# Kernel tuning notes

Measured on AMD Instinct MI355X. Metric: run time of the kernel, lower is better.

Reference implementation:

```python
import jax, jax.numpy as jnp
import numpy as np

IN_F = 4096
OUT_F = 4096
RANK = 16
N_BITS = 4
ALPHA = 1.0
GROUP = 128
Q_N = -(2 ** (N_BITS - 1))       # -8 for 4-bit signed
Q_P = 2 ** (N_BITS - 1) - 1      # +7
EPS = 1e-9


def setup_inputs() -> dict:
    key = jax.random.key(0)
    k0, k1, k2, k3, k4, k5 = jax.random.split(key, 6)
    x = jax.random.normal(k0, (8, 1024, IN_F), dtype=jnp.float32)
    w0 = jax.random.normal(k1, (OUT_F, IN_F), dtype=jnp.float32) * 0.02
    lora_a = jax.random.normal(k2, (RANK, IN_F), dtype=jnp.float32) * 0.02
    lora_b = jax.random.normal(k3, (OUT_F, RANK), dtype=jnp.float32) * 0.02
    num_groups = (OUT_F * IN_F) // GROUP
    q_scale = jnp.abs(jax.random.normal(k4, (num_groups,), dtype=jnp.float32)) * 0.01 + 0.005
    bias = jax.random.normal(k5, (OUT_F,), dtype=jnp.float32) * 0.01
    return {"x": x, "w0": w0, "lora_a": lora_a, "lora_b": lora_b,
            "q_scale": q_scale, "bias": bias}


def _quantize_weight(w0, lora_a, lora_b, q_scale):
    # LoRA merge: w_comb = w0 + alpha * (B @ A)   -> (OUT_F, IN_F)
    w_comb = w0 + ALPHA * (lora_b @ lora_a)
    num_groups = w_comb.size // GROUP
    w_g = w_comb.reshape(num_groups, GROUP)          # grouped view
    s = q_scale[:, None]                             # (G, 1) per-group scale
    w_scaled = w_g / (s + EPS)
    clamped = jnp.clip(w_scaled, Q_N, Q_P)
    q_int = jnp.round(clamped)
    w_q = (q_int * s).reshape(w_comb.shape)          # dequantized fake-quant weight
    return w_q


def reference(x, w0, lora_a, lora_b, q_scale, bias):
    w_q = _quantize_weight(w0, lora_a, lora_b, q_scale)
    # F.linear(x, w_q) + bias : (B, S, IN) @ (IN, OUT)
    return jnp.einsum('bsi,oi->bso', x, w_q) + bias
```

## Files before the change

kernel.cpp:

```cpp
#include <hip/hip_runtime.h>
#include <hip/hip_bf16.h>
#include <stdint.h>
#include <stddef.h>

#define IN_F   4096
#define OUT_F  4096
#define RANK   16
#define GROUP  128
#define M_TOT  8192
#define BM     128
#define BN     128
#define BK     32
#define NIT    (IN_F / BK)

typedef __bf16 bf16_t;
typedef __bf16 bf16x4 __attribute__((ext_vector_type(4)));
typedef __bf16 bf16x8 __attribute__((ext_vector_type(8)));
typedef float  f32x4  __attribute__((ext_vector_type(4)));

__device__ static inline void load_lds16(const void* g, void* l) {
  __builtin_amdgcn_global_load_lds(
      (const __attribute__((address_space(1))) unsigned int*)g,
      (__attribute__((address_space(3))) unsigned int*)l,
      16, 0, 0);
}

__global__ void __launch_bounds__(256)
quant_kernel(const float* __restrict__ w0, const float* __restrict__ la,
             const float* __restrict__ lb, const float* __restrict__ qs,
             bf16_t* __restrict__ wq)
{
  const int o = blockIdx.y;
  const int i = blockIdx.x * 1024 + threadIdx.x * 4;

  __shared__ float lbr[RANK];
  if (threadIdx.x < RANK) lbr[threadIdx.x] = lb[o * RANK + threadIdx.x];
  __syncthreads();

  const size_t off = (size_t)o * IN_F + i;
  const float4 w = *(const float4*)(w0 + off);
  float a0 = w.x, a1 = w.y, a2 = w.z, a3 = w.w;
  #pragma unroll
  for (int r = 0; r < RANK; ++r) {
    const float4 av = *(const float4*)(la + (size_t)r * IN_F + i);
    const float bv = lbr[r];
    a0 = fmaf(bv, av.x, a0);
    a1 = fmaf(bv, av.y, a1);
    a2 = fmaf(bv, av.z, a2);
    a3 = fmaf(bv, av.w, a3);
  }
  const float s   = qs[o * (IN_F / GROUP) + (i >> 7)];
  const float inv = 1.0f / (s + 1e-9f);
  const float q0 = rintf(fminf(fmaxf(a0 * inv, -8.0f), 7.0f)) * s;
  const float q1 = rintf(fminf(fmaxf(a1 * inv, -8.0f), 7.0f)) * s;
  const float q2 = rintf(fminf(fmaxf(a2 * inv, -8.0f), 7.0f)) * s;
  const float q3 = rintf(fminf(fmaxf(a3 * inv, -8.0f), 7.0f)) * s;
  bf16x4 v;
  v[0] = (bf16_t)q0; v[1] = (bf16_t)q1; v[2] = (bf16_t)q2; v[3] = (bf16_t)q3;
  *(bf16x4*)(wq + off) = v;
}

__global__ void __launch_bounds__(256)
castx_kernel(const float* __restrict__ x, bf16_t* __restrict__ xb)
{
  const size_t i = ((size_t)blockIdx.x * 256 + threadIdx.x) * 8;
  const float4 a = *(const float4*)(x + i);
  const float4 b = *(const float4*)(x + i + 4);
  bf16x8 v;
  v[0] = (bf16_t)a.x; v[1] = (bf16_t)a.y; v[2] = (bf16_t)a.z; v[3] = (bf16_t)a.w;
  v[4] = (bf16_t)b.x; v[5] = (bf16_t)b.y; v[6] = (bf16_t)b.z; v[7] = (bf16_t)b.w;
  *(bf16x8*)(xb + i) = v;
}

__global__ void __launch_bounds__(256, 3)
gemm_kernel(const bf16_t* __restrict__ A, const bf16_t* __restrict__ Bw,
            const float* __restrict__ bias, float* __restrict__ C)
{
  __shared__ __align__(16) bf16_t lA[2][BM * BK];
  __shared__ __align__(16) bf16_t lB[2][BN * BK];

  const int tid  = threadIdx.x;
  const int lane = tid & 63;
  const int lr   = lane & 15;
  const int quad = lane >> 4;
  const int wave = tid >> 6;

  const int m0 = blockIdx.y * BM;
  const int n0 = blockIdx.x * BN;

  const int srow = tid >> 2;
  const int scol = (tid & 3) * 8;

  const bf16_t* gA0 = A  + (size_t)(m0 + srow) * IN_F + scol;
  const bf16_t* gA1 = gA0 + (size_t)64 * IN_F;
  const bf16_t* gB0 = Bw + (size_t)(n0 + srow) * IN_F + scol;
  const bf16_t* gB1 = gB0 + (size_t)64 * IN_F;

  const int mb = (wave & 1) * 64;
  const int nb = (wave >> 1) * 64;

  f32x4 acc[4][4];
  #pragma unroll
  for (int i = 0; i < 4; ++i)
    #pragma unroll
    for (int j = 0; j < 4; ++j)
      acc[i][j] = (f32x4){0.f, 0.f, 0.f, 0.f};

  {
    char* dA = (char*)lA[0] + tid * 16;
    char* dB = (char*)lB[0] + tid * 16;
    load_lds16(gA0, dA);
    load_lds16(gA1, dA + 4096);
    load_lds16(gB0, dB);
    load_lds16(gB1, dB + 4096);
  }

  int buf = 0;
  for (int it = 0; it < NIT; ++it) {
    __syncthreads();

    if (it + 1 < NIT) {
      const int kt = (it + 1) * BK;
      char* dA = (char*)lA[buf ^ 1] + tid * 16;
      char* dB = (char*)lB[buf ^ 1] + tid * 16;
      load_lds16(gA0 + kt, dA);
      load_lds16(gA1 + kt, dA + 4096);
      load_lds16(gB0 + kt, dB);
      load_lds16(gB1 + kt, dB + 4096);
    }

    const bf16_t* sA = lA[buf];
    const bf16_t* sB = lB[buf];
    bf16x8 af[4], bfr[4];
    #pragma unroll
    for (int f = 0; f < 4; ++f)
      af[f]  = *(const bf16x8*)(sA + (mb + f * 16 + lr) * BK + quad * 8);
    #pragma unroll
    for (int f = 0; f < 4; ++f)
      bfr[f] = *(const bf16x8*)(sB + (nb + f * 16 + lr) * BK + quad * 8);

    #pragma unroll
    for (int fm = 0; fm < 4; ++fm)
      #pragma unroll
      for (int fn = 0; fn < 4; ++fn)
        acc[fm][fn] = __builtin_amdgcn_mfma_f32_16x16x32_bf16(
            af[fm], bfr[fn], acc[fm][fn], 0, 0, 0);

    buf ^= 1;
  }

  #pragma unroll
  for (int fn = 0; fn < 4; ++fn) {
    const int gn = n0 + nb + fn * 16 + lr;
    const float bv = bias[gn];
    #pragma unroll
    for (int fm = 0; fm < 4; ++fm) {
      const int gm = m0 + mb + fm * 16 + quad * 4;
      #pragma unroll
      for (int r = 0; r < 4; ++r)
        C[(size_t)(gm + r) * OUT_F + gn] = acc[fm][fn][r] + bv;
    }
  }
}

extern "C" void kernel_launch(void* const* d_in, const int* in_sizes, int n_in,
                              void* d_out, int out_size, void* d_ws, size_t ws_size,
                              hipStream_t stream) {
  const float* x    = (const float*)d_in[0];
  const float* w0   = (const float*)d_in[1];
  const float* la   = (const float*)d_in[2];
  const float* lb   = (const float*)d_in[3];
  const float* qs   = (const float*)d_in[4];
  const float* bias = (const float*)d_in[5];
  float* out = (float*)d_out;

  bf16_t* wq = (bf16_t*)d_ws;
  bf16_t* xb = (bf16_t*)((char*)d_ws + (size_t)OUT_F * IN_F * 2);

  quant_kernel<<<dim3(IN_F / 1024, OUT_F), 256, 0, stream>>>(w0, la, lb, qs, wq);
  castx_kernel<<<(M_TOT * IN_F) / (256 * 8), 256, 0, stream>>>(x, xb);
  gemm_kernel<<<dim3(OUT_F / BN, M_TOT / BM), 256, 0, stream>>>(xb, wq, bias, out);
}
```

Baseline: 599.5 us.

## Enlarge GEMM tiles to 256x256 with triple-buffered swizzled LDS pipeline

Reworks the bf16 MFMA GEMM to use 256x256 block tiles with 512 threads (8 waves), a three-stage LDS ring buffer loaded via global_load_lds, XOR-swizzled LDS layout to avoid bank conflicts, and a grid swizzle for L2 locality. The main loop is split into two half-steps, each with explicit waitcnt, barriers and setprio around its MFMA bursts, so global loads overlap compute. This is meant to raise arithmetic intensity and hide memory latency. In exchange it uses 96KB of dynamic LDS, more accumulator registers and hand-tuned synchronisation that could be fragile.

```diff
diff --git a/kernel.cpp b/kernel.cpp
--- a/kernel.cpp
+++ b/kernel.cpp
@@ -8,10 +8,14 @@
 #define RANK   16
 #define GROUP  128
 #define M_TOT  8192
-#define BM     128
-#define BN     128
+
+#define BM     256
+#define BN     256
 #define BK     32
 #define NIT    (IN_F / BK)
+#define HALF_B 16384
+#define TILE_B 32768
+#define LDS_B  (3 * TILE_B)
 
 typedef __bf16 bf16_t;
 typedef __bf16 bf16x4 __attribute__((ext_vector_type(4)));
@@ -72,90 +76,128 @@
   *(bf16x8*)(xb + i) = v;
 }
 
-__global__ void __launch_bounds__(256, 3)
+__global__ void __launch_bounds__(512, 2)
 gemm_kernel(const bf16_t* __restrict__ A, const bf16_t* __restrict__ Bw,
             const float* __restrict__ bias, float* __restrict__ C)
 {
-  __shared__ __align__(16) bf16_t lA[2][BM * BK];
-  __shared__ __align__(16) bf16_t lB[2][BN * BK];
+  extern __shared__ __align__(16) char smem[];
 
   const int tid  = threadIdx.x;
   const int lane = tid & 63;
   const int lr   = lane & 15;
   const int quad = lane >> 4;
-  const int wave = tid >> 6;
-
-  const int m0 = blockIdx.y * BM;
-  const int n0 = blockIdx.x * BN;
+  const int wid  = tid >> 6;
+  const int wm   = wid >> 2;
+  const int wn   = wid & 3;
+
+  const int bid = blockIdx.x;
+  const int swz = (bid & 7) * 64 + (bid >> 3);
+  const int m0  = (swz >> 4) * BM;
+  const int n0  = (swz & 15) * BN;
 
   const int srow = tid >> 2;
-  const int scol = (tid & 3) * 8;
-
+  const int scol = ((tid & 3) ^ ((tid >> 3) & 3)) * 8;
   const bf16_t* gA0 = A  + (size_t)(m0 + srow) * IN_F + scol;
-  const bf16_t* gA1 = gA0 + (size_t)64 * IN_F;
+  const bf16_t* gA1 = gA0 + (size_t)128 * IN_F;
   const bf16_t* gB0 = Bw + (size_t)(n0 + srow) * IN_F + scol;
-  const bf16_t* gB1 = gB0 + (size_t)64 * IN_F;
-
-  const int mb = (wave & 1) * 64;
-  const int nb = (wave >> 1) * 64;
-
-  f32x4 acc[4][4];
+  const bf16_t* gB1 = gB0 + (size_t)128 * IN_F;
+
+  const int rswz = (quad ^ ((lr >> 1) & 3)) * 16;
+  const int aOff = (wm * 128 + lr) * 64 + rswz;
+  const int bOff = (wn * 64  + lr) * 64 + rswz;
+
+  f32x4 acc[8][4];
   #pragma unroll
-  for (int i = 0; i < 4; ++i)
+  for (int i = 0; i < 8; ++i)
     #pragma unroll
     for (int j = 0; j < 4; ++j)
       acc[i][j] = (f32x4){0.f, 0.f, 0.f, 0.f};
 
   {
-    char* dA = (char*)lA[0] + tid * 16;
-    char* dB = (char*)lB[0] + tid * 16;
-    load_lds16(gA0, dA);
-    load_lds16(gA1, dA + 4096);
-    load_lds16(gB0, dB);
-    load_lds16(gB1, dB + 4096);
-  }
-
-  int buf = 0;
-  for (int it = 0; it < NIT; ++it) {
-    __syncthreads();
-
-    if (it + 1 < NIT) {
-      const int kt = (it + 1) * BK;
-      char* dA = (char*)lA[buf ^ 1] + tid * 16;
-      char* dB = (char*)lB[buf ^ 1] + tid * 16;
-      load_lds16(gA0 + kt, dA);
-      load_lds16(gA1 + kt, dA + 4096);
-      load_lds16(gB0 + kt, dB);
-      load_lds16(gB1 + kt, dB + 4096);
+    char* b0 = smem;
+    char* b1 = smem + TILE_B;
+    load_lds16(gA0,      b0 + tid * 16);
+    load_lds16(gA1,      b0 + tid * 16 + 8192);
+    load_lds16(gB0,      b0 + HALF_B + tid * 16);
+    load_lds16(gB1,      b0 + HALF_B + tid * 16 + 8192);
+    load_lds16(gA0 + BK, b1 + tid * 16);
+    load_lds16(gA1 + BK, b1 + tid * 16 + 8192);
+    load_lds16(gB0 + BK, b1 + HALF_B + tid * 16);
+    load_lds16(gB1 + BK, b1 + HALF_B + tid * 16 + 8192);
+    asm volatile("s_waitcnt vmcnt(4)" ::: "memory");
+    __builtin_amdgcn_s_barrier();
+  }
+
+  int rb = 0, wb = 2;
+  for (int t = 0; t < NIT; ++t) {
+    const char* rA   = smem + rb * TILE_B;
+    const char* rB   = rA + HALF_B;
+    char*       wbuf = smem + wb * TILE_B;
+
+    bf16x8 bfr[4];
+    #pragma unroll
+    for (int fn = 0; fn < 4; ++fn)
+      bfr[fn] = *(const bf16x8*)(rB + bOff + fn * 1024);
+    bf16x8 af[4];
+    #pragma unroll
+    for (int f = 0; f < 4; ++f)
+      af[f] = *(const bf16x8*)(rA + aOff + f * 1024);
+
+    if (t + 2 < NIT) {
+      const size_t ko = (size_t)(t + 2) * BK;
+      load_lds16(gA0 + ko, wbuf + tid * 16);
+      load_lds16(gA1 + ko, wbuf + tid * 16 + 8192);
     }
 
-    const bf16_t* sA = lA[buf];
-    const bf16_t* sB = lB[buf];
-    bf16x8 af[4], bfr[4];
-    #pragma unroll
-    for (int f = 0; f < 4; ++f)
-      af[f]  = *(const bf16x8*)(sA + (mb + f * 16 + lr) * BK + quad * 8);
-    #pragma unroll
-    for (int f = 0; f < 4; ++f)
-      bfr[f] = *(const bf16x8*)(sB + (nb + f * 16 + lr) * BK + quad * 8);
-
+    __builtin_amdgcn_s_barrier();
+    asm volatile("s_waitcnt lgkmcnt(0)" ::: "memory");
+    __builtin_amdgcn_sched_barrier(0);
+    __builtin_amdgcn_s_setprio(1);
     #pragma unroll
     for (int fm = 0; fm < 4; ++fm)
       #pragma unroll
       for (int fn = 0; fn < 4; ++fn)
         acc[fm][fn] = __builtin_amdgcn_mfma_f32_16x16x32_bf16(
             af[fm], bfr[fn], acc[fm][fn], 0, 0, 0);
-
-    buf ^= 1;
+    __builtin_amdgcn_s_setprio(0);
+    __builtin_amdgcn_s_barrier();
+
+    #pragma unroll
+    for (int f = 0; f < 4; ++f)
+      af[f] = *(const bf16x8*)(rA + aOff + 4096 + f * 1024);
+
+    if (t + 2 < NIT) {
+      const size_t ko = (size_t)(t + 2) * BK;
+      load_lds16(gB0 + ko, wbuf + HALF_B + tid * 16);
+      load_lds16(gB1 + ko, wbuf + HALF_B + tid * 16 + 8192);
+    }
+
+    if (t + 2 < NIT) asm volatile("s_waitcnt vmcnt(4)" ::: "memory");
+    else             asm volatile("s_waitcnt vmcnt(0)" ::: "memory");
+    __builtin_amdgcn_s_barrier();
+    asm volatile("s_waitcnt lgkmcnt(0)" ::: "memory");
+    __builtin_amdgcn_sched_barrier(0);
+    __builtin_amdgcn_s_setprio(1);
+    #pragma unroll
+    for (int fm = 0; fm < 4; ++fm)
+      #pragma unroll
+      for (int fn = 0; fn < 4; ++fn)
+        acc[4 + fm][fn] = __builtin_amdgcn_mfma_f32_16x16x32_bf16(
+            af[fm], bfr[fn], acc[4 + fm][fn], 0, 0, 0);
+    __builtin_amdgcn_s_setprio(0);
+    __builtin_amdgcn_s_barrier();
+
+    rb = rb + 1; if (rb == 3) rb = 0;
+    wb = wb + 1; if (wb == 3) wb = 0;
   }
 
   #pragma unroll
   for (int fn = 0; fn < 4; ++fn) {
-    const int gn = n0 + nb + fn * 16 + lr;
+    const int gn = n0 + wn * 64 + fn * 16 + lr;
     const float bv = bias[gn];
     #pragma unroll
-    for (int fm = 0; fm < 4; ++fm) {
-      const int gm = m0 + mb + fm * 16 + quad * 4;
+    for (int fm = 0; fm < 8; ++fm) {
+      const int gm = m0 + wm * 128 + fm * 16 + quad * 4;
       #pragma unroll
       for (int r = 0; r < 4; ++r)
         C[(size_t)(gm + r) * OUT_F + gn] = acc[fm][fn][r] + bv;
@@ -177,7 +219,16 @@
   bf16_t* wq = (bf16_t*)d_ws;
   bf16_t* xb = (bf16_t*)((char*)d_ws + (size_t)OUT_F * IN_F * 2);
 
+  static bool attr_done = false;
+  if (!attr_done) {
+    (void)hipFuncSetAttribute((const void*)gemm_kernel,
+                              hipFuncAttributeMaxDynamicSharedMemorySize,
+                              LDS_B);
+    attr_done = true;
+  }
+
   quant_kernel<<<dim3(IN_F / 1024, OUT_F), 256, 0, stream>>>(w0, la, lb, qs, wq);
   castx_kernel<<<(M_TOT * IN_F) / (256 * 8), 256, 0, stream>>>(x, xb);
-  gemm_kernel<<<dim3(OUT_F / BN, M_TOT / BM), 256, 0, stream>>>(xb, wq, bias, out);
-}
+  gemm_kernel<<<dim3((M_TOT / BM) * (OUT_F / BN)), 512, LDS_B, stream>>>(
+      xb, wq, bias, out);
+}
```

Result: faster. 549.6 us (-8.3%).
